# Kernel optimization log

Measured on AMD Instinct MI355X. Metric: run time of the kernel, lower is better.

The kernel has to match this reference:

```python
import jax, jax.numpy as jnp
import numpy as np

LAMDA = 0.05
BETA = 1.0
FULL = 256          # full image / k-space size
SAMP = 128          # sampled k-space size
OFF_R, OFF_C = 3, 3 # sampling offsets from cop.Sample(3, 3, ...)
IR = (OFF_R + 2 * jnp.arange(SAMP)) % FULL  # row sample indices (stride 2)
IC = (OFF_C + 2 * jnp.arange(SAMP)) % FULL  # col sample indices


def dwt2(x):
    # single-level orthonormal 2D Haar DWT, quadrant layout [LL LH; HL HH]
    a = x[..., ::2, ::2]; b = x[..., ::2, 1::2]
    c = x[..., 1::2, ::2]; d = x[..., 1::2, 1::2]
    ll = (a + b + c + d) * 0.5
    lh = (a - b + c - d) * 0.5
    hl = (a + b - c - d) * 0.5
    hh = (a - b - c + d) * 0.5
    top = jnp.concatenate([ll, lh], axis=-1)
    bot = jnp.concatenate([hl, hh], axis=-1)
    return jnp.concatenate([top, bot], axis=-2)


def idwt2(w):
    H = w.shape[-2] // 2; W = w.shape[-1] // 2
    ll = w[..., :H, :W]; lh = w[..., :H, W:]
    hl = w[..., H:, :W]; hh = w[..., H:, W:]
    a = (ll + lh + hl + hh) * 0.5
    b = (ll - lh + hl - hh) * 0.5
    c = (ll + lh - hl - hh) * 0.5
    d = (ll - lh - hl + hh) * 0.5
    x = jnp.zeros(w.shape, w.dtype)
    x = x.at[..., ::2, ::2].set(a)
    x = x.at[..., ::2, 1::2].set(b)
    x = x.at[..., 1::2, ::2].set(c)
    x = x.at[..., 1::2, 1::2].set(d)
    return x


def shrink(x, t):
    # soft-thresholding (prox of t*|x|_1)
    return jnp.sign(x) * jnp.maximum(jnp.abs(x) - t, 0.0)


def sample(x):
    # gather strided k-space samples: [..., 256, 256] -> [..., 128, 128]
    return x[..., IR[:, None], IC[None, :]]


def sample_t(v):
    # adjoint: scatter samples back into zero-filled full grid
    full = jnp.zeros(v.shape[:-2] + (FULL, FULL), v.dtype)
    return full.at[..., IR[:, None], IC[None, :]].set(v)


def setup_inputs() -> dict:
    key = jax.random.key(0)
    k1, k2 = jax.random.split(key)
    s = jax.random.normal(k1, (256, SAMP, SAMP), dtype=jnp.float32)
    image = jax.random.normal(k2, (256, FULL, FULL), dtype=jnp.float32)
    return {"s": s, "image": image}


def reference(s, image):
    thresh = 1.0 / BETA
    coeff = LAMDA / BETA
    dwt_x = dwt2(image)
    new_alpha = shrink(dwt_x, thresh)
    # new_v = dwt_x - new_alpha; idwt(new_alpha - new_v) = idwt(2*alpha - dwt_x)
    idwtx = idwt2(2.0 * new_alpha - dwt_x)
    y = jnp.fft.fft2(idwtx) + coeff * sample_t(s)
    y = y + coeff * sample_t(sample(y))
    return jnp.fft.ifft2(y)
```

## Files before the change

### kernel.cpp

```cpp
#include <hip/hip_runtime.h>


#define NB 128

__device__ __forceinline__ float fwv(float w) {
    float sh = fmaxf(fabsf(w) - 1.0f, 0.0f);
    return 2.0f * copysignf(sh, w) - w;
}

__global__ __launch_bounds__(1024) void fused_kernel(const float* __restrict__ s,
                                                     const float* __restrict__ image,
                                                     float* __restrict__ outf,
                                                     int out_floats)
{
    __shared__ float2 T[128 * NB];

    const int tid = threadIdx.x;
    const int b   = blockIdx.x;
    const float TWO_PI = 6.2831853071795864769f;

    const float* sb = s + (size_t)b * (128 * 128);
    for (int e = tid; e < 128 * 128; e += 1024) {
        int i = e >> 7, j = e & 127;
        int bi = (int)(__builtin_bitreverse32((unsigned)i) >> 25);
        int bj = (int)(__builtin_bitreverse32((unsigned)j) >> 25);
        T[bi * NB + bj] = make_float2(sb[e], 0.0f);
    }
    __syncthreads();

    for (int st = 0; st < 7; ++st) {
        int half = 1 << st;
        for (int bidx = tid; bidx < 8192; bidx += 1024) {
            int row = bidx >> 6;
            int bt  = bidx & 63;
            int r = bt & (half - 1);
            int g = (bt >> st) << (st + 1);
            int i0 = row * NB + g + r;
            int i1 = i0 + half;
            float ws, wc;
            __sincosf(TWO_PI * (float)r / (float)(2 << st), &ws, &wc);
            float2 x0 = T[i0], x1 = T[i1];
            float tr = wc * x1.x - ws * x1.y;
            float ti = wc * x1.y + ws * x1.x;
            T[i0] = make_float2(x0.x + tr, x0.y + ti);
            T[i1] = make_float2(x0.x - tr, x0.y - ti);
        }
        __syncthreads();
    }
    for (int st = 0; st < 7; ++st) {
        int half = 1 << st;
        for (int bidx = tid; bidx < 8192; bidx += 1024) {
            int col = bidx & 127;
            int bt  = bidx >> 7;
            int r = bt & (half - 1);
            int g = (bt >> st) << (st + 1);
            int i0 = (g + r) * NB + col;
            int i1 = i0 + half * NB;
            float ws, wc;
            __sincosf(TWO_PI * (float)r / (float)(2 << st), &ws, &wc);
            float2 x0 = T[i0], x1 = T[i1];
            float tr = wc * x1.x - ws * x1.y;
            float ti = wc * x1.y + ws * x1.x;
            T[i0] = make_float2(x0.x + tr, x0.y + ti);
            T[i1] = make_float2(x0.x - tr, x0.y - ti);
        }
        __syncthreads();
    }

    const float  c0    = 0.0125f;
    const float  kappa = 0.0525f / 65536.0f;
    const size_t obase = (size_t)b * 65536;
    const float2* ib = (const float2*)(image + (size_t)b * 65536);

    for (int qd = tid; qd < 4096; qd += 1024) {
        int p = qd >> 6;
        int q = qd & 63;

        float D[2][2][2][2];
        #pragma unroll
        for (int A = 0; A < 2; ++A) {
            #pragma unroll
            for (int Bq = 0; Bq < 2; ++Bq) {
                int P = p + 64 * A, Q = q + 64 * Bq;
                float2 t0 = ib[(2 * P) * 128 + Q];
                float2 t1 = ib[(2 * P + 1) * 128 + Q];
                float a = t0.x, bb = t0.y, cc = t1.x, dd = t1.y;
                float wll = (a + bb + cc + dd) * 0.5f;
                float wlh = (a - bb + cc - dd) * 0.5f;
                float whl = (a + bb - cc - dd) * 0.5f;
                float whh = (a - bb - cc + dd) * 0.5f;
                float vll = fwv(wll), vlh = fwv(wlh), vhl = fwv(whl), vhh = fwv(whh);
                D[A][Bq][0][0] = (vll + vlh + vhl + vhh) * 0.5f;
                D[A][Bq][0][1] = (vll - vlh + vhl - vhh) * 0.5f;
                D[A][Bq][1][0] = (vll + vlh - vhl - vhh) * 0.5f;
                D[A][Bq][1][1] = (vll - vlh - vhl + vhh) * 0.5f;
            }
        }
        float S[2][2];
        #pragma unroll
        for (int r = 0; r < 2; ++r)
            #pragma unroll
            for (int c = 0; c < 2; ++c)
                S[r][c] = D[0][0][r][c] - D[1][0][r][c] - D[0][1][r][c] + D[1][1][r][c];

        float4 trow0 = *(const float4*)&T[(2 * p) * NB + 2 * q];
        float4 trow1 = *(const float4*)&T[(2 * p + 1) * NB + 2 * q];
        float2 Tv[2][2] = { { make_float2(trow0.x, trow0.y), make_float2(trow0.z, trow0.w) },
                            { make_float2(trow1.x, trow1.y), make_float2(trow1.z, trow1.w) } };

        float2 phv[3];
        #pragma unroll
        for (int k = 0; k < 3; ++k) {
            float ps, pc;
            __sincosf((TWO_PI * 3.0f / 256.0f) * (float)(2 * p + 2 * q + k), &ps, &pc);
            phv[k] = make_float2(pc, ps);
        }

        #pragma unroll
        for (int A = 0; A < 2; ++A) {
            #pragma unroll
            for (int Bq = 0; Bq < 2; ++Bq) {
                float kq  = ((A + Bq) & 1) ? -kappa : kappa;
                float sS  = ((A ^ Bq) & 1) ? -c0 : c0;
                int nrow = 2 * p + 128 * A;
                int mcol = 2 * q + 128 * Bq;
                #pragma unroll
                for (int r = 0; r < 2; ++r) {
                    float2 ph0 = phv[r];
                    float2 ph1 = phv[r + 1];
                    float2 wv;
                    wv.x = D[A][Bq][r][0] + sS * S[r][0]
                         + kq * (ph0.x * Tv[r][0].x - ph0.y * Tv[r][0].y);
                    wv.y = D[A][Bq][r][1] + sS * S[r][1]
                         + kq * (ph1.x * Tv[r][1].x - ph1.y * Tv[r][1].y);
                    size_t fi = obase + (size_t)((nrow + r) * 256 + mcol);
                    if (fi + 2 <= (size_t)out_floats)
                        *(float2*)&outf[fi] = wv;
                }
            }
        }
    }
}

extern "C" void kernel_launch(void* const* d_in, const int* in_sizes, int n_in,
                              void* d_out, int out_size, void* d_ws, size_t ws_size,
                              hipStream_t stream)
{
    const float* s     = (const float*)d_in[0];
    const float* image = (const float*)d_in[1];
    float*       outf  = (float*)d_out;
    hipLaunchKernelGGL(fused_kernel, dim3(256), dim3(1024), 0, stream,
                       s, image, outf, out_size);
}
```

Before: 151.0 us.

## Replace LDS radix-2 FFT stages with register/shuffle-based wavefront FFTs

The 2D 128-point FFT no longer runs as 14 LDS butterfly passes with a barrier after each. Each wavefront now computes whole 128-point row and column FFTs in registers, using DIF butterflies over cross-lane shuffles with twiddles precomputed once per lane. Intermediate results go through a single XOR-swizzled shared-memory transpose, and the final stage reads the bit-reversed output indices. This removes most barriers and per-butterfly sincos and LDS traffic, at the cost of shuffle overhead and more complex indexing.

```diff
diff --git a/kernel.cpp b/kernel.cpp
--- a/kernel.cpp
+++ b/kernel.cpp
@@ -1,11 +1,13 @@
 #include <hip/hip_runtime.h>
 
-
-#define NB 128
 
 __device__ __forceinline__ float fwv(float w) {
     float sh = fmaxf(fabsf(w) - 1.0f, 0.0f);
     return 2.0f * copysignf(sh, w) - w;
+}
+
+__device__ __forceinline__ int bitrev7(int x) {
+    return (int)(__builtin_bitreverse32((unsigned)x) >> 25);
 }
 
 __global__ __launch_bounds__(1024) void fused_kernel(const float* __restrict__ s,
@@ -13,59 +15,70 @@
                                                      float* __restrict__ outf,
                                                      int out_floats)
 {
-    __shared__ float2 T[128 * NB];
+    __shared__ float2 A[128 * 128];
 
-    const int tid = threadIdx.x;
-    const int b   = blockIdx.x;
+    const int tid  = threadIdx.x;
+    const int lane = tid & 63;
+    const int wave = tid >> 6;
+    const int b    = blockIdx.x;
+    const float PI_F   = 3.14159265358979323846f;
     const float TWO_PI = 6.2831853071795864769f;
 
+    float twc[7], tws[7];
+    #pragma unroll
+    for (int k = 0; k < 7; ++k) {
+        int h = 64 >> k;
+        float th = PI_F * (float)(lane & (h - 1)) / (float)h;
+        __sincosf(th, &tws[k], &twc[k]);
+    }
+
+#define FFT128()                                                                     \
+    do {                                                                             \
+        { float ar = x0r, ai = x0i, br = x1r, bi = x1i;                              \
+          x0r = ar + br; x0i = ai + bi;                                              \
+          float dr = ar - br, di = ai - bi;                                          \
+          x1r = dr * twc[0] - di * tws[0];                                           \
+          x1i = dr * tws[0] + di * twc[0]; }                                         \
+        _Pragma("unroll")                                                            \
+        for (int k = 1; k < 7; ++k) {                                                \
+            int h = 64 >> k;                                                         \
+            bool hi = (lane & h) != 0;                                               \
+            float wc = twc[k], ws = tws[k];                                          \
+            { float rr = __shfl_xor(x0r, h), ri = __shfl_xor(x0i, h);                \
+              float sr = hi ? (rr - x0r) : (x0r + rr);                               \
+              float si = hi ? (ri - x0i) : (x0i + ri);                               \
+              float tr = sr * wc - si * ws, ti = sr * ws + si * wc;                  \
+              x0r = hi ? tr : sr; x0i = hi ? ti : si; }                              \
+            { float rr = __shfl_xor(x1r, h), ri = __shfl_xor(x1i, h);                \
+              float sr = hi ? (rr - x1r) : (x1r + rr);                               \
+              float si = hi ? (ri - x1i) : (x1i + ri);                               \
+              float tr = sr * wc - si * ws, ti = sr * ws + si * wc;                  \
+              x1r = hi ? tr : sr; x1i = hi ? ti : si; }                              \
+        }                                                                            \
+    } while (0)
+
     const float* sb = s + (size_t)b * (128 * 128);
-    for (int e = tid; e < 128 * 128; e += 1024) {
-        int i = e >> 7, j = e & 127;
-        int bi = (int)(__builtin_bitreverse32((unsigned)i) >> 25);
-        int bj = (int)(__builtin_bitreverse32((unsigned)j) >> 25);
-        T[bi * NB + bj] = make_float2(sb[e], 0.0f);
+    const int p0 = lane, p1 = 64 | lane;
+    for (int t = 0; t < 8; ++t) {
+        int i = (wave << 3) | t;
+        float x0r = sb[i * 128 + lane],      x0i = 0.0f;
+        float x1r = sb[i * 128 + 64 + lane], x1i = 0.0f;
+        FFT128();
+        A[p0 * 128 + ((i ^ p0) & 127)] = make_float2(x0r, x0i);
+        A[p1 * 128 + ((i ^ p1) & 127)] = make_float2(x1r, x1i);
     }
     __syncthreads();
 
-    for (int st = 0; st < 7; ++st) {
-        int half = 1 << st;
-        for (int bidx = tid; bidx < 8192; bidx += 1024) {
-            int row = bidx >> 6;
-            int bt  = bidx & 63;
-            int r = bt & (half - 1);
-            int g = (bt >> st) << (st + 1);
-            int i0 = row * NB + g + r;
-            int i1 = i0 + half;
-            float ws, wc;
-            __sincosf(TWO_PI * (float)r / (float)(2 << st), &ws, &wc);
-            float2 x0 = T[i0], x1 = T[i1];
-            float tr = wc * x1.x - ws * x1.y;
-            float ti = wc * x1.y + ws * x1.x;
-            T[i0] = make_float2(x0.x + tr, x0.y + ti);
-            T[i1] = make_float2(x0.x - tr, x0.y - ti);
-        }
-        __syncthreads();
+    for (int t = 0; t < 8; ++t) {
+        int vp = (wave << 3) | t;
+        float2 a0 = A[vp * 128 + ((p0 ^ vp) & 127)];
+        float2 a1 = A[vp * 128 + ((p1 ^ vp) & 127)];
+        float x0r = a0.x, x0i = a0.y, x1r = a1.x, x1i = a1.y;
+        FFT128();
+        A[vp * 128 + ((p0 ^ vp) & 127)] = make_float2(x0r, x0i);
+        A[vp * 128 + ((p1 ^ vp) & 127)] = make_float2(x1r, x1i);
     }
-    for (int st = 0; st < 7; ++st) {
-        int half = 1 << st;
-        for (int bidx = tid; bidx < 8192; bidx += 1024) {
-            int col = bidx & 127;
-            int bt  = bidx >> 7;
-            int r = bt & (half - 1);
-            int g = (bt >> st) << (st + 1);
-            int i0 = (g + r) * NB + col;
-            int i1 = i0 + half * NB;
-            float ws, wc;
-            __sincosf(TWO_PI * (float)r / (float)(2 << st), &ws, &wc);
-            float2 x0 = T[i0], x1 = T[i1];
-            float tr = wc * x1.x - ws * x1.y;
-            float ti = wc * x1.y + ws * x1.x;
-            T[i0] = make_float2(x0.x + tr, x0.y + ti);
-            T[i1] = make_float2(x0.x - tr, x0.y - ti);
-        }
-        __syncthreads();
-    }
+    __syncthreads();
 
     const float  c0    = 0.0125f;
     const float  kappa = 0.0525f / 65536.0f;
@@ -78,10 +91,10 @@
 
         float D[2][2][2][2];
         #pragma unroll
-        for (int A = 0; A < 2; ++A) {
+        for (int Aq = 0; Aq < 2; ++Aq) {
             #pragma unroll
             for (int Bq = 0; Bq < 2; ++Bq) {
-                int P = p + 64 * A, Q = q + 64 * Bq;
+                int P = p + 64 * Aq, Q = q + 64 * Bq;
                 float2 t0 = ib[(2 * P) * 128 + Q];
                 float2 t1 = ib[(2 * P + 1) * 128 + Q];
                 float a = t0.x, bb = t0.y, cc = t1.x, dd = t1.y;
@@ -90,10 +103,10 @@
                 float whl = (a + bb - cc - dd) * 0.5f;
                 float whh = (a - bb - cc + dd) * 0.5f;
                 float vll = fwv(wll), vlh = fwv(wlh), vhl = fwv(whl), vhh = fwv(whh);
-                D[A][Bq][0][0] = (vll + vlh + vhl + vhh) * 0.5f;
-                D[A][Bq][0][1] = (vll - vlh + vhl - vhh) * 0.5f;
-                D[A][Bq][1][0] = (vll + vlh - vhl - vhh) * 0.5f;
-                D[A][Bq][1][1] = (vll - vlh - vhl + vhh) * 0.5f;
+                D[Aq][Bq][0][0] = (vll + vlh + vhl + vhh) * 0.5f;
+                D[Aq][Bq][0][1] = (vll - vlh + vhl - vhh) * 0.5f;
+                D[Aq][Bq][1][0] = (vll + vlh - vhl - vhh) * 0.5f;
+                D[Aq][Bq][1][1] = (vll - vlh - vhl + vhh) * 0.5f;
             }
         }
         float S[2][2];
@@ -103,10 +116,13 @@
             for (int c = 0; c < 2; ++c)
                 S[r][c] = D[0][0][r][c] - D[1][0][r][c] - D[0][1][r][c] + D[1][1][r][c];
 
-        float4 trow0 = *(const float4*)&T[(2 * p) * NB + 2 * q];
-        float4 trow1 = *(const float4*)&T[(2 * p + 1) * NB + 2 * q];
-        float2 Tv[2][2] = { { make_float2(trow0.x, trow0.y), make_float2(trow0.z, trow0.w) },
-                            { make_float2(trow1.x, trow1.y), make_float2(trow1.z, trow1.w) } };
+        int ru0 = bitrev7(2 * p), ru1 = bitrev7(2 * p + 1);
+        int rv0 = bitrev7(2 * q), rv1 = bitrev7(2 * q + 1);
+        float2 Tv[2][2];
+        Tv[0][0] = A[rv0 * 128 + ((ru0 ^ rv0) & 127)];
+        Tv[0][1] = A[rv1 * 128 + ((ru0 ^ rv1) & 127)];
+        Tv[1][0] = A[rv0 * 128 + ((ru1 ^ rv0) & 127)];
+        Tv[1][1] = A[rv1 * 128 + ((ru1 ^ rv1) & 127)];
 
         float2 phv[3];
         #pragma unroll
@@ -117,21 +133,21 @@
         }
 
         #pragma unroll
-        for (int A = 0; A < 2; ++A) {
+        for (int Aq = 0; Aq < 2; ++Aq) {
             #pragma unroll
             for (int Bq = 0; Bq < 2; ++Bq) {
-                float kq  = ((A + Bq) & 1) ? -kappa : kappa;
-                float sS  = ((A ^ Bq) & 1) ? -c0 : c0;
-                int nrow = 2 * p + 128 * A;
+                float kq = ((Aq + Bq) & 1) ? -kappa : kappa;
+                float sS = ((Aq ^ Bq) & 1) ? -c0 : c0;
+                int nrow = 2 * p + 128 * Aq;
                 int mcol = 2 * q + 128 * Bq;
                 #pragma unroll
                 for (int r = 0; r < 2; ++r) {
                     float2 ph0 = phv[r];
                     float2 ph1 = phv[r + 1];
                     float2 wv;
-                    wv.x = D[A][Bq][r][0] + sS * S[r][0]
+                    wv.x = D[Aq][Bq][r][0] + sS * S[r][0]
                          + kq * (ph0.x * Tv[r][0].x - ph0.y * Tv[r][0].y);
-                    wv.y = D[A][Bq][r][1] + sS * S[r][1]
+                    wv.y = D[Aq][Bq][r][1] + sS * S[r][1]
                          + kq * (ph1.x * Tv[r][1].x - ph1.y * Tv[r][1].y);
                     size_t fi = obase + (size_t)((nrow + r) * 256 + mcol);
                     if (fi + 2 <= (size_t)out_floats)
@@ -140,6 +156,7 @@
             }
         }
     }
+#undef FFT128
 }
 
 extern "C" void kernel_launch(void* const* d_in, const int* in_sizes, int n_in,
```

New measurement: 142.7 us. -5.5%, faster.
